# Kernel optimization log

Measured on AMD Instinct MI355X. Metric: run time of the kernel, lower is better.

The kernel has to match this reference:

```python
import jax, jax.numpy as jnp
import numpy as np

BN_EPS = 1e-5
N_NODES = 100000
N_EDGES = 1600000
D_IN, D_HID, D_OUT = 128, 128, 64


def _glorot(key, fan_in, fan_out):
    s = jnp.sqrt(6.0 / (fan_in + fan_out))
    return jax.random.uniform(key, (fan_in, fan_out), jnp.float32, -s, s)


def setup_inputs() -> dict:
    key = jax.random.key(0)
    ks = jax.random.split(key, 8)
    x = jax.random.normal(ks[0], (N_NODES, D_IN), jnp.float32)
    edge_index = jax.random.randint(ks[1], (2, N_EDGES), 0, N_NODES, jnp.int64)
    return {
        "x": x,
        "edge_index": edge_index,
        "W1": _glorot(ks[2], D_IN, D_HID), "b1": jnp.zeros(D_HID, jnp.float32),
        "g1": jnp.ones(D_HID, jnp.float32), "be1": jnp.zeros(D_HID, jnp.float32),
        "rm1": jnp.zeros(D_HID, jnp.float32), "rv1": jnp.ones(D_HID, jnp.float32),
        "W2": _glorot(ks[3], D_HID, D_HID), "b2": jnp.zeros(D_HID, jnp.float32),
        "g2": jnp.ones(D_HID, jnp.float32), "be2": jnp.zeros(D_HID, jnp.float32),
        "rm2": jnp.zeros(D_HID, jnp.float32), "rv2": jnp.ones(D_HID, jnp.float32),
        "W3": _glorot(ks[4], D_HID, D_OUT), "b3": jnp.zeros(D_OUT, jnp.float32),
    }


def gcn_conv(x, src, dst, W, b, n):
    """PyG GCNConv: linear, add self-loops, symmetric deg^-1/2 normalization,
    scatter-add aggregation at target nodes, then bias."""
    h = x @ W                                            # [n, d_out]
    # degree with self-loops (unit edge weights)
    deg = jax.ops.segment_sum(jnp.ones(src.shape[0], x.dtype), dst,
                              num_segments=n) + 1.0      # [n]
    dinv = jax.lax.rsqrt(deg)
    norm = dinv[src] * dinv[dst]                         # [E]
    agg = jax.ops.segment_sum(h[src] * norm[:, None], dst, num_segments=n)
    agg = agg + (dinv * dinv)[:, None] * h               # self-loop messages
    return agg + b


def bn_eval(x, gamma, beta, rmean, rvar):
    return (x - rmean) * (gamma * jax.lax.rsqrt(rvar + BN_EPS)) + beta


def reference(x, edge_index, W1, b1, g1, be1, rm1, rv1,
              W2, b2, g2, be2, rm2, rv2, W3, b3):
    src, dst = edge_index[0], edge_index[1]
    n = x.shape[0]
    h = gcn_conv(x, src, dst, W1, b1, n)
    h = jax.nn.relu(bn_eval(h, g1, be1, rm1, rv1))
    h = gcn_conv(h, src, dst, W2, b2, n)
    h = jax.nn.relu(bn_eval(h, g2, be2, rm2, rv2))
    return gcn_conv(h, src, dst, W3, b3, n)
```

## Files before the change

### kernel.cpp

```cpp
#include <hip/hip_runtime.h>


__device__ inline unsigned short f2bf(float f) {
    unsigned int u = __float_as_uint(f);
    u = (u + 0x7FFFu + ((u >> 16) & 1u)) >> 16;
    return (unsigned short)u;
}
__device__ inline float bf_lo(unsigned int u) { return __uint_as_float(u << 16); }
__device__ inline float bf_hi(unsigned int u) { return __uint_as_float(u & 0xFFFF0000u); }

__global__ __launch_bounds__(256) void k_deg(const int* __restrict__ ei,
                                             int* __restrict__ deg,
                                             unsigned short* __restrict__ rank,
                                             int E) {
    int e = blockIdx.x * 256 + threadIdx.x;
    if (e < E)
        rank[e] = (unsigned short)atomicAdd(&deg[ei[E + e]], 1);
}

__global__ __launch_bounds__(256) void k_prep(const int* __restrict__ deg,
                                              float* __restrict__ dinv,
                                              int* __restrict__ degp, int n) {
    int i = blockIdx.x * 256 + threadIdx.x;
    if (i < n) {
        int d = deg[i];
        dinv[i] = rsqrtf((float)d + 1.0f);
        degp[i] = (d + 7) & ~7;
    }
}

__global__ __launch_bounds__(256) void k_scan1(const int* __restrict__ degp,
                                               int* __restrict__ row_ptr,
                                               int* __restrict__ bsums, int n) {
    __shared__ int s[256];
    int i = blockIdx.x * 256 + threadIdx.x;
    int v = (i < n) ? degp[i] : 0;
    s[threadIdx.x] = v;
    __syncthreads();
    for (int off = 1; off < 256; off <<= 1) {
        int add = (threadIdx.x >= off) ? s[threadIdx.x - off] : 0;
        __syncthreads();
        s[threadIdx.x] += add;
        __syncthreads();
    }
    if (i < n) row_ptr[i] = s[threadIdx.x] - v;
    if (threadIdx.x == 255) bsums[blockIdx.x] = s[255];
}

__global__ __launch_bounds__(512) void k_scan2(const int* __restrict__ bsums,
                                               int* __restrict__ boffs, int nb) {
    __shared__ int s[512];
    int t = threadIdx.x;
    int v = (t < nb) ? bsums[t] : 0;
    s[t] = v;
    __syncthreads();
    for (int off = 1; off < 512; off <<= 1) {
        int add = (t >= off) ? s[t - off] : 0;
        __syncthreads();
        s[t] += add;
        __syncthreads();
    }
    if (t < nb) boffs[t] = s[t] - v;
}

__global__ __launch_bounds__(256) void k_scan3(int* __restrict__ row_ptr,
                                               const int* __restrict__ boffs, int n) {
    int i = blockIdx.x * 256 + threadIdx.x;
    if (i < n) row_ptr[i] += boffs[blockIdx.x];
}

__global__ __launch_bounds__(256) void k_fill(const int* __restrict__ ei,
                                              const int* __restrict__ row_ptr,
                                              const unsigned short* __restrict__ rank,
                                              int* __restrict__ csr, int E) {
    int e = blockIdx.x * 256 + threadIdx.x;
    if (e < E) {
        int s = ei[e];
        int d = ei[E + e];
        csr[row_ptr[d] + (int)rank[e]] = s;
    }
}

__global__ __launch_bounds__(256) void k_pad(const int* __restrict__ deg,
                                             const int* __restrict__ degp,
                                             const int* __restrict__ row_ptr,
                                             int* __restrict__ csr, int n) {
    int i = blockIdx.x * 256 + threadIdx.x;
    if (i < n) {
        int start = row_ptr[i];
        int d = deg[i], dp = degp[i];
        for (int j = d; j < dp; ++j) csr[start + j] = n;
    }
}

template <int DOUT>
__global__ __launch_bounds__(256, (DOUT == 128) ? 2 : 4)
void k_gemm(const float* __restrict__ X, const float* __restrict__ W,
            const float* __restrict__ dinv, unsigned short* __restrict__ H,
            int n, int ntiles) {
    constexpr int CG   = DOUT / 4;
    constexpr int ROWS = 1024 / CG;
    __shared__ float Ws[128 * DOUT];

    const int t = threadIdx.x;
    for (int i = t; i < 128 * DOUT; i += 256) Ws[i] = W[i];
    __syncthreads();

    const int tx = t % CG, ty = t / CG;
    const int c0 = tx * 4;

    for (int tile = blockIdx.x; tile < ntiles; tile += gridDim.x) {
        const int rbase = tile * ROWS + ty * 4;
        const float* xr[4];
#pragma unroll
        for (int i = 0; i < 4; i++) {
            int gr = rbase + i;
            xr[i] = X + (size_t)(gr < n ? gr : n - 1) * 128;
        }

        float acc[4][4] = {};
#pragma unroll 2
        for (int k = 0; k < 128; k += 4) {
            float4 xv[4], wv[4];
#pragma unroll
            for (int i = 0; i < 4; i++)
                xv[i] = *(const float4*)(xr[i] + k);
#pragma unroll
            for (int kk = 0; kk < 4; kk++)
                wv[kk] = *(const float4*)&Ws[(k + kk) * DOUT + c0];
#pragma unroll
            for (int kk = 0; kk < 4; kk++) {
                float w0 = wv[kk].x, w1 = wv[kk].y, w2 = wv[kk].z, w3 = wv[kk].w;
#pragma unroll
                for (int i = 0; i < 4; i++) {
                    float xs = (kk == 0) ? xv[i].x
                             : (kk == 1) ? xv[i].y
                             : (kk == 2) ? xv[i].z
                                         : xv[i].w;
                    acc[i][0] = fmaf(xs, w0, acc[i][0]);
                    acc[i][1] = fmaf(xs, w1, acc[i][1]);
                    acc[i][2] = fmaf(xs, w2, acc[i][2]);
                    acc[i][3] = fmaf(xs, w3, acc[i][3]);
                }
            }
        }
#pragma unroll
        for (int i = 0; i < 4; i++) {
            int gr = rbase + i;
            if (gr < n) {
                float di = dinv[gr];
                ushort4 s;
                s.x = f2bf(di * acc[i][0]);
                s.y = f2bf(di * acc[i][1]);
                s.z = f2bf(di * acc[i][2]);
                s.w = f2bf(di * acc[i][3]);
                *(ushort4*)&H[(size_t)gr * DOUT + c0] = s;
            }
        }
    }
}

template <int DOUT, bool BNRELU>
__global__ __launch_bounds__(256) void k_agg(
    const unsigned short* __restrict__ Hs, float* __restrict__ O,
    const int* __restrict__ csr, const int* __restrict__ row_ptr,
    const int* __restrict__ degp, const float* __restrict__ dinv,
    const float* __restrict__ bias, const float* __restrict__ gam,
    const float* __restrict__ bet, const float* __restrict__ rm,
    const float* __restrict__ rv, int n) {
    int node = blockIdx.x * 4 + (threadIdx.x >> 6);
    if (node >= n) return;
    int lane  = threadIdx.x & 63;
    int start = row_ptr[node];
    int cntp  = degp[node];
    float di  = dinv[node];
    const unsigned int* Hu = (const unsigned int*)Hs;

    if constexpr (DOUT == 128) {
        const int c = lane;
        unsigned int us = Hu[(size_t)node * 64 + c];
        float2 a[8];
        a[0] = make_float2(bf_lo(us), bf_hi(us));
#pragma unroll
        for (int j = 1; j < 8; j++) a[j] = make_float2(0.f, 0.f);
        for (int e = 0; e < cntp; e += 8) {
            int4 sa = *(const int4*)&csr[start + e];
            int4 sb = *(const int4*)&csr[start + e + 4];
            unsigned int u0 = Hu[(size_t)sa.x * 64 + c];
            unsigned int u1 = Hu[(size_t)sa.y * 64 + c];
            unsigned int u2 = Hu[(size_t)sa.z * 64 + c];
            unsigned int u3 = Hu[(size_t)sa.w * 64 + c];
            unsigned int u4 = Hu[(size_t)sb.x * 64 + c];
            unsigned int u5 = Hu[(size_t)sb.y * 64 + c];
            unsigned int u6 = Hu[(size_t)sb.z * 64 + c];
            unsigned int u7 = Hu[(size_t)sb.w * 64 + c];
            a[0].x += bf_lo(u0); a[0].y += bf_hi(u0);
            a[1].x += bf_lo(u1); a[1].y += bf_hi(u1);
            a[2].x += bf_lo(u2); a[2].y += bf_hi(u2);
            a[3].x += bf_lo(u3); a[3].y += bf_hi(u3);
            a[4].x += bf_lo(u4); a[4].y += bf_hi(u4);
            a[5].x += bf_lo(u5); a[5].y += bf_hi(u5);
            a[6].x += bf_lo(u6); a[6].y += bf_hi(u6);
            a[7].x += bf_lo(u7); a[7].y += bf_hi(u7);
        }
        float ax = ((a[0].x + a[1].x) + (a[2].x + a[3].x)) +
                   ((a[4].x + a[5].x) + (a[6].x + a[7].x));
        float ay = ((a[0].y + a[1].y) + (a[2].y + a[3].y)) +
                   ((a[4].y + a[5].y) + (a[6].y + a[7].y));
        int cc = 2 * c;
        float ox = fmaf(di, ax, bias[cc]);
        float oy = fmaf(di, ay, bias[cc + 1]);
        if constexpr (BNRELU) {
            float sx = gam[cc] * rsqrtf(rv[cc] + 1e-5f);
            float sy = gam[cc + 1] * rsqrtf(rv[cc + 1] + 1e-5f);
            ox = fmaxf(fmaf(ox - rm[cc], sx, bet[cc]), 0.f);
            oy = fmaxf(fmaf(oy - rm[cc + 1], sy, bet[cc + 1]), 0.f);
        }
        *(float2*)(O + (size_t)node * 128 + cc) = make_float2(ox, oy);
    } else {
        const int half = lane >> 5, cu = lane & 31;
        float2 a0 = {0.f, 0.f}, a1 = {0.f, 0.f}, a2 = {0.f, 0.f}, a3 = {0.f, 0.f};
        for (int e = 0; e < cntp; e += 8) {
            int4 sa = *(const int4*)&csr[start + e];
            int4 sb = *(const int4*)&csr[start + e + 4];
            int i0 = half ? sa.y : sa.x;
            int i1 = half ? sa.w : sa.z;
            int i2 = half ? sb.y : sb.x;
            int i3 = half ? sb.w : sb.z;
            unsigned int u0 = Hu[(size_t)i0 * 32 + cu];
            unsigned int u1 = Hu[(size_t)i1 * 32 + cu];
            unsigned int u2 = Hu[(size_t)i2 * 32 + cu];
            unsigned int u3 = Hu[(size_t)i3 * 32 + cu];
            a0.x += bf_lo(u0); a0.y += bf_hi(u0);
            a1.x += bf_lo(u1); a1.y += bf_hi(u1);
            a2.x += bf_lo(u2); a2.y += bf_hi(u2);
            a3.x += bf_lo(u3); a3.y += bf_hi(u3);
        }
        float sx = (a0.x + a1.x) + (a2.x + a3.x);
        float sy = (a0.y + a1.y) + (a2.y + a3.y);
        sx += __shfl_xor(sx, 32, 64);
        sy += __shfl_xor(sy, 32, 64);
        if (half == 0) {
            unsigned int us = Hu[(size_t)node * 32 + cu];
            sx += bf_lo(us);
            sy += bf_hi(us);
            int cc = 2 * cu;
            float ox = fmaf(di, sx, bias[cc]);
            float oy = fmaf(di, sy, bias[cc + 1]);
            *(float2*)(O + (size_t)node * 64 + cc) = make_float2(ox, oy);
        }
    }
}

extern "C" void kernel_launch(void* const* d_in, const int* in_sizes, int n_in,
                              void* d_out, int out_size, void* d_ws, size_t ws_size,
                              hipStream_t stream) {
    const float* x   = (const float*)d_in[0];
    const int*   ei  = (const int*)d_in[1];
    const float* W1  = (const float*)d_in[2];
    const float* b1  = (const float*)d_in[3];
    const float* g1  = (const float*)d_in[4];
    const float* be1 = (const float*)d_in[5];
    const float* rm1 = (const float*)d_in[6];
    const float* rv1 = (const float*)d_in[7];
    const float* W2  = (const float*)d_in[8];
    const float* b2  = (const float*)d_in[9];
    const float* g2  = (const float*)d_in[10];
    const float* be2 = (const float*)d_in[11];
    const float* rm2 = (const float*)d_in[12];
    const float* rv2 = (const float*)d_in[13];
    const float* W3  = (const float*)d_in[14];
    const float* b3  = (const float*)d_in[15];

    const int n = in_sizes[0] / 128;
    const int E = in_sizes[1] / 2;

    char*  w   = (char*)d_ws;
    size_t off = 0;
    auto take  = [&](size_t bytes) -> char* {
        char* p = w + off;
        off += (bytes + 255) & ~(size_t)255;
        return p;
    };
    int*   deg    = (int*)take((size_t)n * 4);
    int*   degp   = (int*)take((size_t)n * 4);
    int*   rowp   = (int*)take((size_t)n * 4);
    float* dinv   = (float*)take((size_t)n * 4);
    unsigned short* rank = (unsigned short*)take((size_t)E * 2);
    const int NB  = (n + 255) / 256;
    int*   bsums  = (int*)take((size_t)NB * 4);
    int*   boffs  = (int*)take((size_t)NB * 4);
    int*   csr    = (int*)take((size_t)E * 4 + (size_t)n * 7 * 4 + 64);
    unsigned short* Hs = (unsigned short*)take(((size_t)n + 1) * 128 * 2);
    float* Of     = (float*)take((size_t)n * 128 * 4);
    (void)ws_size; (void)n_in; (void)out_size;

    hipMemsetAsync(deg, 0, (size_t)n * 4, stream);
    const int egrid = (E + 255) / 256;
    k_deg<<<egrid, 256, 0, stream>>>(ei, deg, rank, E);
    k_prep<<<NB, 256, 0, stream>>>(deg, dinv, degp, n);
    k_scan1<<<NB, 256, 0, stream>>>(degp, rowp, bsums, n);
    k_scan2<<<1, 512, 0, stream>>>(bsums, boffs, NB);
    k_scan3<<<NB, 256, 0, stream>>>(rowp, boffs, n);
    k_fill<<<egrid, 256, 0, stream>>>(ei, rowp, rank, csr, E);
    k_pad<<<NB, 256, 0, stream>>>(deg, degp, rowp, csr, n);
    hipMemsetAsync((char*)Hs + (size_t)n * 256, 0, 256, stream);

    const int nt128 = (n + 31) / 32;
    const int nt64  = (n + 63) / 64;
    const int g128  = nt128 < 512 ? nt128 : 512;
    const int g64   = nt64 < 512 ? nt64 : 512;
    const int agrid = (n + 3) / 4;

    k_gemm<128><<<g128, 256, 0, stream>>>(x, W1, dinv, Hs, n, nt128);
    k_agg<128, true><<<agrid, 256, 0, stream>>>(Hs, Of, csr, rowp, degp, dinv,
                                                b1, g1, be1, rm1, rv1, n);
    k_gemm<128><<<g128, 256, 0, stream>>>(Of, W2, dinv, Hs, n, nt128);
    k_agg<128, true><<<agrid, 256, 0, stream>>>(Hs, Of, csr, rowp, degp, dinv,
                                                b2, g2, be2, rm2, rv2, n);
    k_gemm<64><<<g64, 256, 0, stream>>>(Of, W3, dinv, Hs, n, nt64);
    hipMemsetAsync((char*)Hs + (size_t)n * 128, 0, 128, stream);
    k_agg<64, false><<<agrid, 256, 0, stream>>>(Hs, (float*)d_out, csr, rowp, degp,
                                                dinv, b3, nullptr, nullptr, nullptr,
                                                nullptr, n);
}
```

Before: 568.2 us.

## Replace FP32 FMA GEMM with split-bf16 MFMA GEMM and bf16 hi/lo activations

```diff
diff --git a/kernel.cpp b/kernel.cpp
--- a/kernel.cpp
+++ b/kernel.cpp
@@ -1,10 +1,19 @@
 #include <hip/hip_runtime.h>
 
+
+typedef short     bf16x8 __attribute__((ext_vector_type(8)));
+typedef float     f32x4  __attribute__((ext_vector_type(4)));
+typedef unsigned short us8 __attribute__((ext_vector_type(8)));
+typedef unsigned short us4 __attribute__((ext_vector_type(4)));
+typedef unsigned short us2 __attribute__((ext_vector_type(2)));
 
 __device__ inline unsigned short f2bf(float f) {
     unsigned int u = __float_as_uint(f);
     u = (u + 0x7FFFu + ((u >> 16) & 1u)) >> 16;
     return (unsigned short)u;
+}
+__device__ inline float bf2f(unsigned short h) {
+    return __uint_as_float(((unsigned int)h) << 16);
 }
 __device__ inline float bf_lo(unsigned int u) { return __uint_as_float(u << 16); }
 __device__ inline float bf_hi(unsigned int u) { return __uint_as_float(u & 0xFFFF0000u); }
@@ -93,68 +102,124 @@
     }
 }
 
-template <int DOUT>
-__global__ __launch_bounds__(256, (DOUT == 128) ? 2 : 4)
-void k_gemm(const float* __restrict__ X, const float* __restrict__ W,
-            const float* __restrict__ dinv, unsigned short* __restrict__ H,
-            int n, int ntiles) {
-    constexpr int CG   = DOUT / 4;
-    constexpr int ROWS = 1024 / CG;
-    __shared__ float Ws[128 * DOUT];
-
-    const int t = threadIdx.x;
-    for (int i = t; i < 128 * DOUT; i += 256) Ws[i] = W[i];
-    __syncthreads();
-
-    const int tx = t % CG, ty = t / CG;
-    const int c0 = tx * 4;
-
-    for (int tile = blockIdx.x; tile < ntiles; tile += gridDim.x) {
-        const int rbase = tile * ROWS + ty * 4;
-        const float* xr[4];
-#pragma unroll
-        for (int i = 0; i < 4; i++) {
-            int gr = rbase + i;
-            xr[i] = X + (size_t)(gr < n ? gr : n - 1) * 128;
-        }
-
-        float acc[4][4] = {};
-#pragma unroll 2
-        for (int k = 0; k < 128; k += 4) {
-            float4 xv[4], wv[4];
-#pragma unroll
-            for (int i = 0; i < 4; i++)
-                xv[i] = *(const float4*)(xr[i] + k);
-#pragma unroll
-            for (int kk = 0; kk < 4; kk++)
-                wv[kk] = *(const float4*)&Ws[(k + kk) * DOUT + c0];
+template <int N>
+__global__ __launch_bounds__(256) void k_wprep(const float* __restrict__ W,
+                                               unsigned short* __restrict__ WhT,
+                                               unsigned short* __restrict__ WlT) {
+    int tid = blockIdx.x * 256 + threadIdx.x;
+    if (tid < 128 * N) {
+        int k = tid / N, c = tid % N;
+        float v = W[tid];
+        unsigned short h = f2bf(v);
+        unsigned short l = f2bf(v - bf2f(h));
+        WhT[c * 128 + k] = h;
+        WlT[c * 128 + k] = l;
+    }
+}
+
+template <int DOUT, bool FP32IN>
+__global__ __launch_bounds__(256, 3)
+void k_gemm_mfma(const float* __restrict__ Xf,
+                 const unsigned short* __restrict__ Xhg,
+                 const unsigned short* __restrict__ Xlg,
+                 const unsigned short* __restrict__ WhT,
+                 const unsigned short* __restrict__ WlT,
+                 const float* __restrict__ dinv,
+                 unsigned short* __restrict__ H, int n, int nrt) {
+    constexpr int CH = DOUT / 64;
+    __shared__ unsigned short Xh[32 * 136], Xl[32 * 136];
+    __shared__ unsigned short Wh[64 * 136], Wl[64 * 136];
+
+    const int t  = threadIdx.x;
+    const int ch = (CH == 2) ? (blockIdx.x & 1) : 0;
+
+#pragma unroll
+    for (int i = 0; i < 4; i++) {
+        int c = t + i * 256;
+        int row = c >> 4, s = c & 15;
+        *(us8*)&Wh[row * 136 + s * 8] =
+            *(const us8*)&WhT[(ch * 64 + row) * 128 + s * 8];
+        *(us8*)&Wl[row * 136 + s * 8] =
+            *(const us8*)&WlT[(ch * 64 + row) * 128 + s * 8];
+    }
+
+    const int lane = t & 63;
+    const int w    = t >> 6;
+    const int wrow = (w >> 1) * 16;
+    const int wcol = (w & 1) * 32;
+    const int arow = wrow + (lane & 15);
+    const int koff = (lane >> 4) * 8;
+
+    const int rt0    = (CH == 2) ? (blockIdx.x >> 1) : blockIdx.x;
+    const int rtstep = (CH == 2) ? (gridDim.x >> 1) : gridDim.x;
+
+    for (int rt = rt0; rt < nrt; rt += rtstep) {
+        const int rbase = rt * 32;
+        __syncthreads();
+
+        if constexpr (FP32IN) {
+#pragma unroll
+            for (int i = 0; i < 4; i++) {
+                int c = t + i * 256;
+                int row = c >> 5, s4 = c & 31;
+                int gr = rbase + row;
+                float4 v = *(const float4*)&Xf[(size_t)(gr < n ? gr : n - 1) * 128 + s4 * 4];
+                us4 h, l;
+                h.x = f2bf(v.x); l.x = f2bf(v.x - bf2f(h.x));
+                h.y = f2bf(v.y); l.y = f2bf(v.y - bf2f(h.y));
+                h.z = f2bf(v.z); l.z = f2bf(v.z - bf2f(h.z));
+                h.w = f2bf(v.w); l.w = f2bf(v.w - bf2f(h.w));
+                *(us4*)&Xh[row * 136 + s4 * 4] = h;
+                *(us4*)&Xl[row * 136 + s4 * 4] = l;
+            }
+        } else {
+#pragma unroll
+            for (int i = 0; i < 2; i++) {
+                int c = t + i * 256;
+                int row = c >> 4, s = c & 15;
+                int gr = rbase + row;
+                size_t gb = (size_t)(gr < n ? gr : n - 1) * 128 + s * 8;
+                *(us8*)&Xh[row * 136 + s * 8] = *(const us8*)&Xhg[gb];
+                *(us8*)&Xl[row * 136 + s * 8] = *(const us8*)&Xlg[gb];
+            }
+        }
+        __syncthreads();
+
+        bf16x8 ah[4], al[4];
+#pragma unroll
+        for (int kk = 0; kk < 4; kk++) {
+            ah[kk] = *(const bf16x8*)&Xh[arow * 136 + kk * 32 + koff];
+            al[kk] = *(const bf16x8*)&Xl[arow * 136 + kk * 32 + koff];
+        }
+
+        f32x4 acc[2];
+#pragma unroll
+        for (int f = 0; f < 2; f++) {
+            const int col = wcol + f * 16 + (lane & 15);
+            bf16x8 bh[4], bl[4];
 #pragma unroll
             for (int kk = 0; kk < 4; kk++) {
-                float w0 = wv[kk].x, w1 = wv[kk].y, w2 = wv[kk].z, w3 = wv[kk].w;
-#pragma unroll
-                for (int i = 0; i < 4; i++) {
-                    float xs = (kk == 0) ? xv[i].x
-                             : (kk == 1) ? xv[i].y
-                             : (kk == 2) ? xv[i].z
-                                         : xv[i].w;
-                    acc[i][0] = fmaf(xs, w0, acc[i][0]);
-                    acc[i][1] = fmaf(xs, w1, acc[i][1]);
-                    acc[i][2] = fmaf(xs, w2, acc[i][2]);
-                    acc[i][3] = fmaf(xs, w3, acc[i][3]);
-                }
+                bh[kk] = *(const bf16x8*)&Wh[col * 136 + kk * 32 + koff];
+                bl[kk] = *(const bf16x8*)&Wl[col * 136 + kk * 32 + koff];
             }
-        }
-#pragma unroll
-        for (int i = 0; i < 4; i++) {
-            int gr = rbase + i;
-            if (gr < n) {
-                float di = dinv[gr];
-                ushort4 s;
-                s.x = f2bf(di * acc[i][0]);
-                s.y = f2bf(di * acc[i][1]);
-                s.z = f2bf(di * acc[i][2]);
-                s.w = f2bf(di * acc[i][3]);
-                *(ushort4*)&H[(size_t)gr * DOUT + c0] = s;
+            f32x4 a = {0.f, 0.f, 0.f, 0.f};
+#pragma unroll
+            for (int kk = 0; kk < 4; kk++) {
+                a = __builtin_amdgcn_mfma_f32_16x16x32_bf16(ah[kk], bh[kk], a, 0, 0, 0);
+                a = __builtin_amdgcn_mfma_f32_16x16x32_bf16(ah[kk], bl[kk], a, 0, 0, 0);
+                a = __builtin_amdgcn_mfma_f32_16x16x32_bf16(al[kk], bh[kk], a, 0, 0, 0);
+            }
+            acc[f] = a;
+        }
+
+#pragma unroll
+        for (int r = 0; r < 4; r++) {
+            int row = rbase + wrow + (lane >> 4) * 4 + r;
+            if (row < n) {
+                float dv = dinv[row];
+                int cb = ch * 64 + wcol + (lane & 15);
+                H[(size_t)row * DOUT + cb]      = f2bf(dv * acc[0][r]);
+                H[(size_t)row * DOUT + cb + 16] = f2bf(dv * acc[1][r]);
             }
         }
     }
@@ -162,7 +227,9 @@
 
 template <int DOUT, bool BNRELU>
 __global__ __launch_bounds__(256) void k_agg(
-    const unsigned short* __restrict__ Hs, float* __restrict__ O,
+    const unsigned short* __restrict__ Hs,
+    unsigned short* __restrict__ XhB, unsigned short* __restrict__ XlB,
+    float* __restrict__ O,
     const int* __restrict__ csr, const int* __restrict__ row_ptr,
     const int* __restrict__ degp, const float* __restrict__ dinv,
     const float* __restrict__ bias, const float* __restrict__ gam,
@@ -216,7 +283,11 @@
             ox = fmaxf(fmaf(ox - rm[cc], sx, bet[cc]), 0.f);
             oy = fmaxf(fmaf(oy - rm[cc + 1], sy, bet[cc + 1]), 0.f);
         }
-        *(float2*)(O + (size_t)node * 128 + cc) = make_float2(ox, oy);
+        us2 h, l;
+        h.x = f2bf(ox); l.x = f2bf(ox - bf2f(h.x));
+        h.y = f2bf(oy); l.y = f2bf(oy - bf2f(h.y));
+        *(us2*)&XhB[(size_t)node * 128 + cc] = h;
+        *(us2*)&XlB[(size_t)node * 128 + cc] = l;
     } else {
         const int half = lane >> 5, cu = lane & 31;
         float2 a0 = {0.f, 0.f}, a1 = {0.f, 0.f}, a2 = {0.f, 0.f}, a3 = {0.f, 0.f};
@@ -291,8 +362,15 @@
     int*   bsums  = (int*)take((size_t)NB * 4);
     int*   boffs  = (int*)take((size_t)NB * 4);
     int*   csr    = (int*)take((size_t)E * 4 + (size_t)n * 7 * 4 + 64);
-    unsigned short* Hs = (unsigned short*)take(((size_t)n + 1) * 128 * 2);
-    float* Of     = (float*)take((size_t)n * 128 * 4);
+    unsigned short* Hs  = (unsigned short*)take(((size_t)n + 1) * 128 * 2);
+    unsigned short* Xh  = (unsigned short*)take((size_t)n * 128 * 2);
+    unsigned short* Xl  = (unsigned short*)take((size_t)n * 128 * 2);
+    unsigned short* Wh1 = (unsigned short*)take(128 * 128 * 2);
+    unsigned short* Wl1 = (unsigned short*)take(128 * 128 * 2);
+    unsigned short* Wh2 = (unsigned short*)take(128 * 128 * 2);
+    unsigned short* Wl2 = (unsigned short*)take(128 * 128 * 2);
+    unsigned short* Wh3 = (unsigned short*)take(64 * 128 * 2);
+    unsigned short* Wl3 = (unsigned short*)take(64 * 128 * 2);
     (void)ws_size; (void)n_in; (void)out_size;
 
     hipMemsetAsync(deg, 0, (size_t)n * 4, stream);
@@ -306,21 +384,25 @@
     k_pad<<<NB, 256, 0, stream>>>(deg, degp, rowp, csr, n);
     hipMemsetAsync((char*)Hs + (size_t)n * 256, 0, 256, stream);
 
-    const int nt128 = (n + 31) / 32;
-    const int nt64  = (n + 63) / 64;
-    const int g128  = nt128 < 512 ? nt128 : 512;
-    const int g64   = nt64 < 512 ? nt64 : 512;
+    k_wprep<128><<<64, 256, 0, stream>>>(W1, Wh1, Wl1);
+    k_wprep<128><<<64, 256, 0, stream>>>(W2, Wh2, Wl2);
+    k_wprep<64><<<32, 256, 0, stream>>>(W3, Wh3, Wl3);
+
+    const int nrt   = (n + 31) / 32;
     const int agrid = (n + 3) / 4;
 
-    k_gemm<128><<<g128, 256, 0, stream>>>(x, W1, dinv, Hs, n, nt128);
-    k_agg<128, true><<<agrid, 256, 0, stream>>>(Hs, Of, csr, rowp, degp, dinv,
-                                                b1, g1, be1, rm1, rv1, n);
-    k_gemm<128><<<g128, 256, 0, stream>>>(Of, W2, dinv, Hs, n, nt128);
-    k_agg<128, true><<<agrid, 256, 0, stream>>>(Hs, Of, csr, rowp, degp, dinv,
-                                                b2, g2, be2, rm2, rv2, n);
-    k_gemm<64><<<g64, 256, 0, stream>>>(Of, W3, dinv, Hs, n, nt64);
+    k_gemm_mfma<128, true><<<512, 256, 0, stream>>>(x, nullptr, nullptr,
+                                                    Wh1, Wl1, dinv, Hs, n, nrt);
+    k_agg<128, true><<<agrid, 256, 0, stream>>>(Hs, Xh, Xl, nullptr, csr, rowp,
+                                                degp, dinv, b1, g1, be1, rm1, rv1, n);
+    k_gemm_mfma<128, false><<<512, 256, 0, stream>>>(nullptr, Xh, Xl,
+                                                     Wh2, Wl2, dinv, Hs, n, nrt);
+    k_agg<128, true><<<agrid, 256, 0, stream>>>(Hs, Xh, Xl, nullptr, csr, rowp,
+                                                degp, dinv, b2, g2, be2, rm2, rv2, n);
+    k_gemm_mfma<64, false><<<512, 256, 0, stream>>>(nullptr, Xh, Xl,
+                                                    Wh3, Wl3, dinv, Hs, n, nrt);
     hipMemsetAsync((char*)Hs + (size_t)n * 128, 0, 128, stream);
-    k_agg<64, false><<<agrid, 256, 0, stream>>>(Hs, (float*)d_out, csr, rowp, degp,
-                                                dinv, b3, nullptr, nullptr, nullptr,
-                                                nullptr, n);
-}
+    k_agg<64, false><<<agrid, 256, 0, stream>>>(Hs, nullptr, nullptr, (float*)d_out,
+                                                csr, rowp, degp, dinv, b3, nullptr,
+                                                nullptr, nullptr, nullptr, n);
+}
```

New measurement: 482.6 us. 1.18x faster.
